# Optimization experiments

Measured on AMD Instinct MI355X. Metric: run time of the kernel, lower is better.

Reference implementation:

```python
import jax, jax.numpy as jnp
import numpy as np

WINDOW_SIZE = 512
CAUSAL = True

def _sliding_window_mask(seq_len, window_size, causal):
    i = jnp.arange(seq_len)[:, None]
    j = jnp.arange(seq_len)[None, :]
    mask = (j >= i - window_size + 1) & (j <= i)
    if causal:
        mask = mask & (j <= i)
    return mask  # [S, S] bool, True = attend


def setup_inputs() -> dict:
    key = jax.random.key(0)
    k1, k2, k3 = jax.random.split(key, 3)
    B, S, D = 16, 4096, 64
    q = jax.random.normal(k1, (B, S, D), dtype=jnp.float32)
    k = jax.random.normal(k2, (B, S, D), dtype=jnp.float32)
    v = jax.random.normal(k3, (B, S, D), dtype=jnp.float32)
    return {"q": q, "k": k, "v": v}


def reference(q, k, v):
    B, S, D = q.shape
    scale = D ** -0.5
    mask = _sliding_window_mask(S, WINDOW_SIZE, CAUSAL)  # [S, S]
    scores = jnp.einsum("bqd,bkd->bqk", q, k) * scale    # [B, S, S]
    mask_value = -jnp.finfo(scores.dtype).max
    scores = jnp.where(mask[None, :, :], scores, mask_value)
    attn = jax.nn.softmax(scores, axis=-1)
    out = jnp.einsum("bqk,bkd->bqd", attn, v)            # [B, S, D]
    return out
```

## Files before the change

kernel.cpp:

```cpp
#include <hip/hip_runtime.h>

#define BATCH 16
#define SEQ   4096
#define DIM   64
#define WIN   512

constexpr int BM = 64;
constexpr int BN = 64;
constexpr int NTHREADS = 256;
constexpr int NTILES = SEQ / BN;
constexpr int TILEB  = 8192;
constexpr int BUFB   = 2 * TILEB;
constexpr int SMEMB  = 2 * BUFB;

constexpr float QSCALE  = 0.125f * 1.44269504088896340736f;
constexpr float MASKVAL = -3.0e38f;
constexpr float DEFER_THR = 8.0f;

typedef _Float16 f16x2 __attribute__((ext_vector_type(2)));
typedef _Float16 f16x4 __attribute__((ext_vector_type(4)));
typedef _Float16 f16x8 __attribute__((ext_vector_type(8)));
typedef float    f32x4 __attribute__((ext_vector_type(4)));

__device__ __forceinline__ f16x2 pk2(float a, float b) {
    return __builtin_bit_cast(f16x2, __builtin_amdgcn_cvt_pkrtz(a, b));
}

__device__ __forceinline__ void gl16(const char* g, char* l) {
    __builtin_amdgcn_global_load_lds(
        (const __attribute__((address_space(1))) unsigned int*)g,
        (__attribute__((address_space(3))) unsigned int*)l, 16, 0, 0);
}

__global__ __launch_bounds__(256)
void prep_kernel(const float* __restrict__ kg, const float* __restrict__ vg,
                 _Float16* __restrict__ k16, _Float16* __restrict__ vt16) {
    const int t    = threadIdx.x;
    const int b    = blockIdx.y;
    const int tile = blockIdx.x;
    const int s0   = tile * 64;

    {
        const int rb    = t >> 4;
        const int c4    = (t & 15) * 4;
        const int chunk = c4 >> 3;
        const int half  = (c4 >> 2) & 1;
        char* kout = (char*)k16 + ((size_t)b * NTILES + tile) * TILEB;
        #pragma unroll
        for (int i = 0; i < 4; ++i) {
            const int row = rb + i * 16;
            const float4 x = *(const float4*)&kg[((size_t)b * SEQ + s0 + row) * DIM + c4];
            union { f16x4 v; f16x2 h[2]; } u;
            u.h[0] = pk2(x.x, x.y); u.h[1] = pk2(x.z, x.w);
            *(f16x4*)(kout + row * 128 + ((chunk ^ (row & 7)) << 4) + half * 8) = u.v;
        }
    }
    {
        const int d   = t >> 2;
        const int j   = t & 3;
        const int swz = (j ^ ((d >> 2) & 3)) << 3;
        char* vout = (char*)vt16 + ((size_t)b * NTILES + tile) * TILEB;
        #pragma unroll
        for (int p = 0; p < 4; ++p) {
            const size_t kr = (size_t)b * SEQ + s0 + p * 16 + 4 * j;
            const float x0 = vg[(kr + 0) * DIM + d];
            const float x1 = vg[(kr + 1) * DIM + d];
            const float x2 = vg[(kr + 2) * DIM + d];
            const float x3 = vg[(kr + 3) * DIM + d];
            union { f16x4 v; f16x2 h[2]; } u;
            u.h[0] = pk2(x0, x1); u.h[1] = pk2(x2, x3);
            *(f16x4*)(vout + p * 2048 + d * 32 + swz) = u.v;
        }
    }
}

__global__ __launch_bounds__(NTHREADS, 4)
void swa_main(const float* __restrict__ qg, float* __restrict__ outg,
              const _Float16* __restrict__ k16, const _Float16* __restrict__ vt16) {
    __shared__ __align__(16) char smem[SMEMB];

    const int tid  = threadIdx.x;
    const int lane = tid & 63;
    const int wave = tid >> 6;
    const int lr   = lane & 15;
    const int quad = lane >> 4;

    static_assert(SEQ / BM == 64 && BATCH == 16, "swizzle assumes 1024 blocks");
    const int lin    = blockIdx.x;
    const int xcd    = lin & 7;
    const int slot   = lin >> 3;
    const int member = slot & 7;
    const int gchunk = (slot >> 3) * 8 + xcd;
    const int b      = gchunk >> 3;
    const int qblk   = (gchunk & 7) * 8 + member;

    const int qrow0 = qblk * BM;
    const int wr0   = qrow0 + wave * 16;
    const int q     = wr0 + lr;

    const float* qb  = qg + (size_t)b * SEQ * DIM;
    float*       ob  = outg + (size_t)b * SEQ * DIM;
    const char*  kbb = (const char*)k16 + (size_t)b * NTILES * TILEB;
    const char*  vbb = (const char*)vt16 + (size_t)b * NTILES * TILEB;

    const int kaddr0 = lr * 128 + (((quad    ) ^ (lr & 7)) << 4);
    const int kaddr1 = lr * 128 + (((quad + 4) ^ (lr & 7)) << 4);
    const int vaddr  = lr * 32 + ((quad ^ (lr >> 2)) << 3);
    const int dmaoff = wave * 1024 + lane * 16;
    char* const ldsw = smem;

    const float* qp = qb + (size_t)q * DIM + quad * 8;
    const float4 a0 = *(const float4*)(qp + 0);
    const float4 a1 = *(const float4*)(qp + 4);
    const float4 a2 = *(const float4*)(qp + 32);
    const float4 a3 = *(const float4*)(qp + 36);
    union { f16x8 v; f16x2 h[4]; } uq0, uq1;
    uq0.h[0] = pk2(a0.x * QSCALE, a0.y * QSCALE);
    uq0.h[1] = pk2(a0.z * QSCALE, a0.w * QSCALE);
    uq0.h[2] = pk2(a1.x * QSCALE, a1.y * QSCALE);
    uq0.h[3] = pk2(a1.z * QSCALE, a1.w * QSCALE);
    uq1.h[0] = pk2(a2.x * QSCALE, a2.y * QSCALE);
    uq1.h[1] = pk2(a2.z * QSCALE, a2.w * QSCALE);
    uq1.h[2] = pk2(a3.x * QSCALE, a3.y * QSCALE);
    uq1.h[3] = pk2(a3.z * QSCALE, a3.w * QSCALE);
    const f16x8 qf0 = uq0.v, qf1 = uq1.v;

    f32x4 o[4];
    #pragma unroll
    for (int mi = 0; mi < 4; ++mi) o[mi] = (f32x4){0.f, 0.f, 0.f, 0.f};
    float m_run = -1e30f, l_run = 0.f;

    const int t0 = (qrow0 > (WIN - 1)) ? (qrow0 - (WIN - 1)) >> 6 : 0;
    const int t1 = (qrow0 + BM - 1) >> 6;

    {
        const char* gK = kbb + (size_t)t0 * TILEB;
        const char* gV = vbb + (size_t)t0 * TILEB;
        gl16(gK + dmaoff,        ldsw + wave * 1024);
        gl16(gK + dmaoff + 4096, ldsw + wave * 1024 + 4096);
        gl16(gV + dmaoff,        ldsw + TILEB + wave * 1024);
        gl16(gV + dmaoff + 4096, ldsw + TILEB + wave * 1024 + 4096);
    }
    __syncthreads();

    for (int t = t0; t <= t1; ++t) {
        const int cb = (t - t0) & 1;
        const char* Kc = smem + cb * BUFB;
        const char* Vc = Kc + TILEB;

        if (t < t1) {
            char* nb = ldsw + (cb ^ 1) * BUFB;
            const char* gK = kbb + (size_t)(t + 1) * TILEB;
            const char* gV = vbb + (size_t)(t + 1) * TILEB;
            gl16(gK + dmaoff,        nb + wave * 1024);
            gl16(gK + dmaoff + 4096, nb + wave * 1024 + 4096);
            gl16(gV + dmaoff,        nb + TILEB + wave * 1024);
            gl16(gV + dmaoff + 4096, nb + TILEB + wave * 1024 + 4096);
        }

        const int kbase = t * BN;
        const int u     = (wr0 - kbase) >> 4;
        const int mtlo  = (u - 32 > 0) ? u - 32 : 0;
        const int mthi  = (u < 3) ? u : 3;

        if (mtlo <= mthi) {
            f32x4 sc[4];
            #pragma unroll
            for (int mt = 0; mt < 4; ++mt) {
                if (mt >= mtlo && mt <= mthi) {
                    const f16x8 kf0 = *(const f16x8*)(Kc + mt * 2048 + kaddr0);
                    const f16x8 kf1 = *(const f16x8*)(Kc + mt * 2048 + kaddr1);
                    f32x4 s = (f32x4){0.f, 0.f, 0.f, 0.f};
                    s = __builtin_amdgcn_mfma_f32_16x16x32_f16(kf0, qf0, s, 0, 0, 0);
                    s = __builtin_amdgcn_mfma_f32_16x16x32_f16(kf1, qf1, s, 0, 0, 0);
                    sc[mt] = s;
                }
            }

            const bool edge = (kbase + mtlo * 16 < wr0 + 15 - (WIN - 1)) ||
                              (kbase + mthi * 16 + 15 > wr0);
            if (edge) {
                #pragma unroll
                for (int mt = 0; mt < 4; ++mt) {
                    if (mt >= mtlo && mt <= mthi) {
                        #pragma unroll
                        for (int r = 0; r < 4; ++r) {
                            const int key = kbase + mt * 16 + quad * 4 + r;
                            sc[mt][r] = ((unsigned)(q - key) < (unsigned)WIN) ? sc[mt][r] : MASKVAL;
                        }
                    }
                }
            }

            float pm = MASKVAL;
            #pragma unroll
            for (int mt = 0; mt < 4; ++mt) {
                if (mt >= mtlo && mt <= mthi) {
                    pm = fmaxf(pm, fmaxf(fmaxf(sc[mt][0], sc[mt][1]),
                                         fmaxf(sc[mt][2], sc[mt][3])));
                }
            }
            if (__any(pm > m_run + DEFER_THR)) {
                float pmf = pm;
                pmf = fmaxf(pmf, __shfl_xor(pmf, 16));
                pmf = fmaxf(pmf, __shfl_xor(pmf, 32));
                const float mn    = fmaxf(m_run, pmf);
                const float alpha = exp2f(m_run - mn);
                m_run = mn;
                l_run *= alpha;
                #pragma unroll
                for (int mi = 0; mi < 4; ++mi) o[mi] = o[mi] * alpha;
            }

            f16x4 pb[4];
            float ls = 0.f;
            #pragma unroll
            for (int nt = 0; nt < 4; ++nt) {
                if (nt >= mtlo && nt <= mthi) {
                    const float p0 = exp2f(sc[nt][0] - m_run);
                    const float p1 = exp2f(sc[nt][1] - m_run);
                    const float p2 = exp2f(sc[nt][2] - m_run);
                    const float p3 = exp2f(sc[nt][3] - m_run);
                    ls += (p0 + p1) + (p2 + p3);
                    union { f16x4 v; f16x2 h[2]; } up;
                    up.h[0] = pk2(p0, p1);
                    up.h[1] = pk2(p2, p3);
                    pb[nt] = up.v;
                }
            }
            l_run += ls;

            #pragma unroll
            for (int nt = 0; nt < 4; ++nt) {
                if (nt >= mtlo && nt <= mthi) {
                    #pragma unroll
                    for (int mi = 0; mi < 4; ++mi) {
                        const f16x4 vf = *(const f16x4*)(Vc + nt * 2048 + mi * 512 + vaddr);
                        o[mi] = __builtin_amdgcn_mfma_f32_16x16x16f16(vf, pb[nt], o[mi], 0, 0, 0);
                    }
                }
            }
        }

        __syncthreads();
    }

    l_run += __shfl_xor(l_run, 16);
    l_run += __shfl_xor(l_run, 32);
    const float inv = 1.0f / l_run;
    #pragma unroll
    for (int mi = 0; mi < 4; ++mi) {
        float4 st;
        st.x = o[mi][0] * inv; st.y = o[mi][1] * inv;
        st.z = o[mi][2] * inv; st.w = o[mi][3] * inv;
        *(float4*)&ob[(size_t)q * DIM + mi * 16 + quad * 4] = st;
    }
}

extern "C" void kernel_launch(void* const* d_in, const int* in_sizes, int n_in,
                              void* d_out, int out_size, void* d_ws, size_t ws_size,
                              hipStream_t stream) {
    (void)in_sizes; (void)n_in; (void)out_size; (void)ws_size;
    const float* q = (const float*)d_in[0];
    const float* k = (const float*)d_in[1];
    const float* v = (const float*)d_in[2];
    float* out = (float*)d_out;

    const size_t KVB = (size_t)BATCH * SEQ * DIM * sizeof(_Float16);
    _Float16* vt16 = (_Float16*)d_ws;
    _Float16* k16  = (_Float16*)((char*)d_ws + KVB);

    prep_kernel<<<dim3(NTILES, BATCH), dim3(256), 0, stream>>>(k, v, k16, vt16);
    swa_main<<<dim3(BATCH * SEQ / BM), dim3(NTHREADS), 0, stream>>>(q, out, k16, vt16);
}
```

Baseline: 116.0 us.

## Process two 16-row query groups per wave with 128-thread blocks

Each wave now handles 32 query rows (two 16-row MFMA groups) instead of 16, so every K and V fragment read from LDS feeds two MFMAs. Blocks shrink to 2 waves, and each wave issues more async global-to-LDS copies per tile. This aims to cut LDS read traffic per FLOP and raise MFMA density. In exchange it doubles accumulator and score registers per thread, which may lower occupancy, and halves the number of waves available to hide latency.

```diff
diff --git a/kernel.cpp b/kernel.cpp
--- a/kernel.cpp
+++ b/kernel.cpp
@@ -7,7 +7,7 @@
 
 constexpr int BM = 64;
 constexpr int BN = 64;
-constexpr int NTHREADS = 256;
+constexpr int NTHREADS = 128;
 constexpr int NTILES = SEQ / BN;
 constexpr int TILEB  = 8192;
 constexpr int BUFB   = 2 * TILEB;
@@ -74,7 +74,7 @@
     }
 }
 
-__global__ __launch_bounds__(NTHREADS, 4)
+__global__ __launch_bounds__(NTHREADS, 2)
 void swa_main(const float* __restrict__ qg, float* __restrict__ outg,
               const _Float16* __restrict__ k16, const _Float16* __restrict__ vt16) {
     __shared__ __align__(16) char smem[SMEMB];
@@ -95,8 +95,9 @@
     const int qblk   = (gchunk & 7) * 8 + member;
 
     const int qrow0 = qblk * BM;
-    const int wr0   = qrow0 + wave * 16;
-    const int q     = wr0 + lr;
+    const int wr0   = qrow0 + wave * 32;
+    const int q0    = wr0 + lr;
+    const int q1    = wr0 + 16 + lr;
 
     const float* qb  = qg + (size_t)b * SEQ * DIM;
     float*       ob  = outg + (size_t)b * SEQ * DIM;
@@ -106,29 +107,51 @@
     const int kaddr0 = lr * 128 + (((quad    ) ^ (lr & 7)) << 4);
     const int kaddr1 = lr * 128 + (((quad + 4) ^ (lr & 7)) << 4);
     const int vaddr  = lr * 32 + ((quad ^ (lr >> 2)) << 3);
-    const int dmaoff = wave * 1024 + lane * 16;
-    char* const ldsw = smem;
-
-    const float* qp = qb + (size_t)q * DIM + quad * 8;
-    const float4 a0 = *(const float4*)(qp + 0);
-    const float4 a1 = *(const float4*)(qp + 4);
-    const float4 a2 = *(const float4*)(qp + 32);
-    const float4 a3 = *(const float4*)(qp + 36);
-    union { f16x8 v; f16x2 h[4]; } uq0, uq1;
-    uq0.h[0] = pk2(a0.x * QSCALE, a0.y * QSCALE);
-    uq0.h[1] = pk2(a0.z * QSCALE, a0.w * QSCALE);
-    uq0.h[2] = pk2(a1.x * QSCALE, a1.y * QSCALE);
-    uq0.h[3] = pk2(a1.z * QSCALE, a1.w * QSCALE);
-    uq1.h[0] = pk2(a2.x * QSCALE, a2.y * QSCALE);
-    uq1.h[1] = pk2(a2.z * QSCALE, a2.w * QSCALE);
-    uq1.h[2] = pk2(a3.x * QSCALE, a3.y * QSCALE);
-    uq1.h[3] = pk2(a3.z * QSCALE, a3.w * QSCALE);
-    const f16x8 qf0 = uq0.v, qf1 = uq1.v;
-
-    f32x4 o[4];
+    const int dmaoff = wave * 4096 + lane * 16;
+
+    f16x8 qfA0, qfA1, qfB0, qfB1;
+    {
+        const float* qp = qb + (size_t)q0 * DIM + quad * 8;
+        const float4 a0 = *(const float4*)(qp + 0);
+        const float4 a1 = *(const float4*)(qp + 4);
+        const float4 a2 = *(const float4*)(qp + 32);
+        const float4 a3 = *(const float4*)(qp + 36);
+        union { f16x8 v; f16x2 h[4]; } u0, u1;
+        u0.h[0] = pk2(a0.x * QSCALE, a0.y * QSCALE);
+        u0.h[1] = pk2(a0.z * QSCALE, a0.w * QSCALE);
+        u0.h[2] = pk2(a1.x * QSCALE, a1.y * QSCALE);
+        u0.h[3] = pk2(a1.z * QSCALE, a1.w * QSCALE);
+        u1.h[0] = pk2(a2.x * QSCALE, a2.y * QSCALE);
+        u1.h[1] = pk2(a2.z * QSCALE, a2.w * QSCALE);
+        u1.h[2] = pk2(a3.x * QSCALE, a3.y * QSCALE);
+        u1.h[3] = pk2(a3.z * QSCALE, a3.w * QSCALE);
+        qfA0 = u0.v; qfA1 = u1.v;
+    }
+    {
+        const float* qp = qb + (size_t)q1 * DIM + quad * 8;
+        const float4 a0 = *(const float4*)(qp + 0);
+        const float4 a1 = *(const float4*)(qp + 4);
+        const float4 a2 = *(const float4*)(qp + 32);
+        const float4 a3 = *(const float4*)(qp + 36);
+        union { f16x8 v; f16x2 h[4]; } u0, u1;
+        u0.h[0] = pk2(a0.x * QSCALE, a0.y * QSCALE);
+        u0.h[1] = pk2(a0.z * QSCALE, a0.w * QSCALE);
+        u0.h[2] = pk2(a1.x * QSCALE, a1.y * QSCALE);
+        u0.h[3] = pk2(a1.z * QSCALE, a1.w * QSCALE);
+        u1.h[0] = pk2(a2.x * QSCALE, a2.y * QSCALE);
+        u1.h[1] = pk2(a2.z * QSCALE, a2.w * QSCALE);
+        u1.h[2] = pk2(a3.x * QSCALE, a3.y * QSCALE);
+        u1.h[3] = pk2(a3.z * QSCALE, a3.w * QSCALE);
+        qfB0 = u0.v; qfB1 = u1.v;
+    }
+
+    f32x4 o0[4], o1[4];
     #pragma unroll
-    for (int mi = 0; mi < 4; ++mi) o[mi] = (f32x4){0.f, 0.f, 0.f, 0.f};
-    float m_run = -1e30f, l_run = 0.f;
+    for (int mi = 0; mi < 4; ++mi) {
+        o0[mi] = (f32x4){0.f, 0.f, 0.f, 0.f};
+        o1[mi] = (f32x4){0.f, 0.f, 0.f, 0.f};
+    }
+    float m0 = -1e30f, l0 = 0.f, m1 = -1e30f, l1 = 0.f;
 
     const int t0 = (qrow0 > (WIN - 1)) ? (qrow0 - (WIN - 1)) >> 6 : 0;
     const int t1 = (qrow0 + BM - 1) >> 6;
@@ -136,10 +159,11 @@
     {
         const char* gK = kbb + (size_t)t0 * TILEB;
         const char* gV = vbb + (size_t)t0 * TILEB;
-        gl16(gK + dmaoff,        ldsw + wave * 1024);
-        gl16(gK + dmaoff + 4096, ldsw + wave * 1024 + 4096);
-        gl16(gV + dmaoff,        ldsw + TILEB + wave * 1024);
-        gl16(gV + dmaoff + 4096, ldsw + TILEB + wave * 1024 + 4096);
+        #pragma unroll
+        for (int c = 0; c < 4; ++c) {
+            gl16(gK + dmaoff + c * 1024, smem + wave * 4096 + lane * 16 + c * 1024);
+            gl16(gV + dmaoff + c * 1024, smem + TILEB + wave * 4096 + lane * 16 + c * 1024);
+        }
     }
     __syncthreads();
 
@@ -149,36 +173,41 @@
         const char* Vc = Kc + TILEB;
 
         if (t < t1) {
-            char* nb = ldsw + (cb ^ 1) * BUFB;
+            char* nb = smem + (cb ^ 1) * BUFB;
             const char* gK = kbb + (size_t)(t + 1) * TILEB;
             const char* gV = vbb + (size_t)(t + 1) * TILEB;
-            gl16(gK + dmaoff,        nb + wave * 1024);
-            gl16(gK + dmaoff + 4096, nb + wave * 1024 + 4096);
-            gl16(gV + dmaoff,        nb + TILEB + wave * 1024);
-            gl16(gV + dmaoff + 4096, nb + TILEB + wave * 1024 + 4096);
+            #pragma unroll
+            for (int c = 0; c < 4; ++c) {
+                gl16(gK + dmaoff + c * 1024, nb + wave * 4096 + lane * 16 + c * 1024);
+                gl16(gV + dmaoff + c * 1024, nb + TILEB + wave * 4096 + lane * 16 + c * 1024);
+            }
         }
 
         const int kbase = t * BN;
         const int u     = (wr0 - kbase) >> 4;
         const int mtlo  = (u - 32 > 0) ? u - 32 : 0;
-        const int mthi  = (u < 3) ? u : 3;
+        const int mthi  = (u + 1 < 3) ? u + 1 : 3;
 
         if (mtlo <= mthi) {
-            f32x4 sc[4];
+            f32x4 sc0[4], sc1[4];
             #pragma unroll
             for (int mt = 0; mt < 4; ++mt) {
                 if (mt >= mtlo && mt <= mthi) {
                     const f16x8 kf0 = *(const f16x8*)(Kc + mt * 2048 + kaddr0);
                     const f16x8 kf1 = *(const f16x8*)(Kc + mt * 2048 + kaddr1);
                     f32x4 s = (f32x4){0.f, 0.f, 0.f, 0.f};
-                    s = __builtin_amdgcn_mfma_f32_16x16x32_f16(kf0, qf0, s, 0, 0, 0);
-                    s = __builtin_amdgcn_mfma_f32_16x16x32_f16(kf1, qf1, s, 0, 0, 0);
-                    sc[mt] = s;
-                }
-            }
-
-            const bool edge = (kbase + mtlo * 16 < wr0 + 15 - (WIN - 1)) ||
-                              (kbase + mthi * 16 + 15 > wr0);
+                    s = __builtin_amdgcn_mfma_f32_16x16x32_f16(kf0, qfA0, s, 0, 0, 0);
+                    s = __builtin_amdgcn_mfma_f32_16x16x32_f16(kf1, qfA1, s, 0, 0, 0);
+                    sc0[mt] = s;
+                    f32x4 r = (f32x4){0.f, 0.f, 0.f, 0.f};
+                    r = __builtin_amdgcn_mfma_f32_16x16x32_f16(kf0, qfB0, r, 0, 0, 0);
+                    r = __builtin_amdgcn_mfma_f32_16x16x32_f16(kf1, qfB1, r, 0, 0, 0);
+                    sc1[mt] = r;
+                }
+            }
+
+            const bool edge = ((wr0 + 31) - (kbase + mtlo * 16) >= WIN) ||
+                              ((kbase + mthi * 16 + 15) > wr0);
             if (edge) {
                 #pragma unroll
                 for (int mt = 0; mt < 4; ++mt) {
@@ -186,49 +215,80 @@
                         #pragma unroll
                         for (int r = 0; r < 4; ++r) {
                             const int key = kbase + mt * 16 + quad * 4 + r;
-                            sc[mt][r] = ((unsigned)(q - key) < (unsigned)WIN) ? sc[mt][r] : MASKVAL;
+                            sc0[mt][r] = ((unsigned)(q0 - key) < (unsigned)WIN) ? sc0[mt][r] : MASKVAL;
+                            sc1[mt][r] = ((unsigned)(q1 - key) < (unsigned)WIN) ? sc1[mt][r] : MASKVAL;
                         }
                     }
                 }
             }
 
-            float pm = MASKVAL;
-            #pragma unroll
-            for (int mt = 0; mt < 4; ++mt) {
-                if (mt >= mtlo && mt <= mthi) {
-                    pm = fmaxf(pm, fmaxf(fmaxf(sc[mt][0], sc[mt][1]),
-                                         fmaxf(sc[mt][2], sc[mt][3])));
-                }
-            }
-            if (__any(pm > m_run + DEFER_THR)) {
-                float pmf = pm;
-                pmf = fmaxf(pmf, __shfl_xor(pmf, 16));
-                pmf = fmaxf(pmf, __shfl_xor(pmf, 32));
-                const float mn    = fmaxf(m_run, pmf);
-                const float alpha = exp2f(m_run - mn);
-                m_run = mn;
-                l_run *= alpha;
-                #pragma unroll
-                for (int mi = 0; mi < 4; ++mi) o[mi] = o[mi] * alpha;
-            }
-
-            f16x4 pb[4];
-            float ls = 0.f;
-            #pragma unroll
-            for (int nt = 0; nt < 4; ++nt) {
-                if (nt >= mtlo && nt <= mthi) {
-                    const float p0 = exp2f(sc[nt][0] - m_run);
-                    const float p1 = exp2f(sc[nt][1] - m_run);
-                    const float p2 = exp2f(sc[nt][2] - m_run);
-                    const float p3 = exp2f(sc[nt][3] - m_run);
-                    ls += (p0 + p1) + (p2 + p3);
-                    union { f16x4 v; f16x2 h[2]; } up;
-                    up.h[0] = pk2(p0, p1);
-                    up.h[1] = pk2(p2, p3);
-                    pb[nt] = up.v;
-                }
-            }
-            l_run += ls;
+            f16x4 pb0[4], pb1[4];
+            {
+                float pm = MASKVAL;
+                #pragma unroll
+                for (int mt = 0; mt < 4; ++mt)
+                    if (mt >= mtlo && mt <= mthi)
+                        pm = fmaxf(pm, fmaxf(fmaxf(sc0[mt][0], sc0[mt][1]),
+                                             fmaxf(sc0[mt][2], sc0[mt][3])));
+                if (__any(pm > m0 + DEFER_THR)) {
+                    float pmf = fmaxf(pm, __shfl_xor(pm, 16));
+                    pmf = fmaxf(pmf, __shfl_xor(pmf, 32));
+                    const float mn    = fmaxf(m0, pmf);
+                    const float alpha = exp2f(m0 - mn);
+                    m0 = mn; l0 *= alpha;
+                    #pragma unroll
+                    for (int mi = 0; mi < 4; ++mi) o0[mi] = o0[mi] * alpha;
+                }
+                float ls = 0.f;
+                #pragma unroll
+                for (int nt = 0; nt < 4; ++nt) {
+                    if (nt >= mtlo && nt <= mthi) {
+                        const float p0 = exp2f(sc0[nt][0] - m0);
+                        const float p1 = exp2f(sc0[nt][1] - m0);
+                        const float p2 = exp2f(sc0[nt][2] - m0);
+                        const float p3 = exp2f(sc0[nt][3] - m0);
+                        ls += (p0 + p1) + (p2 + p3);
+                        union { f16x4 v; f16x2 h[2]; } up;
+                        up.h[0] = pk2(p0, p1);
+                        up.h[1] = pk2(p2, p3);
+                        pb0[nt] = up.v;
+                    }
+                }
+                l0 += ls;
+            }
+            {
+                float pm = MASKVAL;
+                #pragma unroll
+                for (int mt = 0; mt < 4; ++mt)
+                    if (mt >= mtlo && mt <= mthi)
+                        pm = fmaxf(pm, fmaxf(fmaxf(sc1[mt][0], sc1[mt][1]),
+                                             fmaxf(sc1[mt][2], sc1[mt][3])));
+                if (__any(pm > m1 + DEFER_THR)) {
+                    float pmf = fmaxf(pm, __shfl_xor(pm, 16));
+                    pmf = fmaxf(pmf, __shfl_xor(pmf, 32));
+                    const float mn    = fmaxf(m1, pmf);
+                    const float alpha = exp2f(m1 - mn);
+                    m1 = mn; l1 *= alpha;
+                    #pragma unroll
+                    for (int mi = 0; mi < 4; ++mi) o1[mi] = o1[mi] * alpha;
+                }
+                float ls = 0.f;
+                #pragma unroll
+                for (int nt = 0; nt < 4; ++nt) {
+                    if (nt >= mtlo && nt <= mthi) {
+                        const float p0 = exp2f(sc1[nt][0] - m1);
+                        const float p1 = exp2f(sc1[nt][1] - m1);
+                        const float p2 = exp2f(sc1[nt][2] - m1);
+                        const float p3 = exp2f(sc1[nt][3] - m1);
+                        ls += (p0 + p1) + (p2 + p3);
+                        union { f16x4 v; f16x2 h[2]; } up;
+                        up.h[0] = pk2(p0, p1);
+                        up.h[1] = pk2(p2, p3);
+                        pb1[nt] = up.v;
+                    }
+                }
+                l1 += ls;
+            }
 
             #pragma unroll
             for (int nt = 0; nt < 4; ++nt) {
@@ -236,7 +296,8 @@
                     #pragma unroll
                     for (int mi = 0; mi < 4; ++mi) {
                         const f16x4 vf = *(const f16x4*)(Vc + nt * 2048 + mi * 512 + vaddr);
-                        o[mi] = __builtin_amdgcn_mfma_f32_16x16x16f16(vf, pb[nt], o[mi], 0, 0, 0);
+                        o0[mi] = __builtin_amdgcn_mfma_f32_16x16x16f16(vf, pb0[nt], o0[mi], 0, 0, 0);
+                        o1[mi] = __builtin_amdgcn_mfma_f32_16x16x16f16(vf, pb1[nt], o1[mi], 0, 0, 0);
                     }
                 }
             }
@@ -245,15 +306,31 @@
         __syncthreads();
     }
 
-    l_run += __shfl_xor(l_run, 16);
-    l_run += __shfl_xor(l_run, 32);
-    const float inv = 1.0f / l_run;
-    #pragma unroll
-    for (int mi = 0; mi < 4; ++mi) {
-        float4 st;
-        st.x = o[mi][0] * inv; st.y = o[mi][1] * inv;
-        st.z = o[mi][2] * inv; st.w = o[mi][3] * inv;
-        *(float4*)&ob[(size_t)q * DIM + mi * 16 + quad * 4] = st;
+    {
+        float l = l0;
+        l += __shfl_xor(l, 16);
+        l += __shfl_xor(l, 32);
+        const float inv = 1.0f / l;
+        #pragma unroll
+        for (int mi = 0; mi < 4; ++mi) {
+            float4 st;
+            st.x = o0[mi][0] * inv; st.y = o0[mi][1] * inv;
+            st.z = o0[mi][2] * inv; st.w = o0[mi][3] * inv;
+            *(float4*)&ob[(size_t)q0 * DIM + mi * 16 + quad * 4] = st;
+        }
+    }
+    {
+        float l = l1;
+        l += __shfl_xor(l, 16);
+        l += __shfl_xor(l, 32);
+        const float inv = 1.0f / l;
+        #pragma unroll
+        for (int mi = 0; mi < 4; ++mi) {
+            float4 st;
+            st.x = o1[mi][0] * inv; st.y = o1[mi][1] * inv;
+            st.z = o1[mi][2] * inv; st.w = o1[mi][3] * inv;
+            *(float4*)&ob[(size_t)q1 * DIM + mi * 16 + quad * 4] = st;
+        }
     }
 }
 
```

After: 121.1 us. 4.4% more time.
